# Performance work log

Measured on AMD Instinct MI355X. Metric: run time of the kernel, lower is better.

The kernel has to match this reference:

```python
import jax, jax.numpy as jnp
import numpy as np

BATCH, DIM, DB_SIZE, TOP_K = 2048, 512, 50000, 5

def setup_inputs() -> dict:
    key = jax.random.key(0)
    k1, k2 = jax.random.split(key)
    h_current = jax.random.normal(k1, (BATCH, DIM), dtype=jnp.float32)
    history_db = jax.random.normal(k2, (DB_SIZE, DIM), dtype=jnp.float32) * 0.01
    alpha = jnp.float32(0.5)
    return {"h_current": h_current, "history_db": history_db, "alpha": alpha, "top_k": TOP_K}

def _l2_normalize(x, eps=1e-12):
    # matches F.normalize(p=2): x / max(||x||, eps)
    n = jnp.linalg.norm(x, axis=-1, keepdims=True)
    return x / jnp.maximum(n, eps)

def reference(h_current, history_db, alpha, top_k):
    h_norm = _l2_normalize(h_current)            # (B, D)
    db_norm = _l2_normalize(history_db)          # (M, D)
    similarity = h_norm @ db_norm.T              # (B, M)
    topk_sim, topk_idx = jax.lax.top_k(similarity, top_k)  # (B, K)
    mu = jax.nn.softmax(topk_sim, axis=-1)       # (B, K)
    topk_embeddings = history_db[topk_idx]       # (B, K, D)
    h_retrieved = jnp.einsum('bk,bkd->bd', mu, topk_embeddings)
    a = jax.nn.sigmoid(alpha)
    return a * h_current + (1.0 - a) * h_retrieved
```

## Files before the change

### kernel.cpp

```cpp
#include <hip/hip_runtime.h>

#define BATCH   2048
#define DIM     512
#define DB_N    50000
#define TOPK    5
#define PADN    50176
#define NCHUNK  56
#define CTILES  7
#define CCOLS   896
#define TM      128
#define TN      128
#define NFIN    12

typedef float f32x4 __attribute__((ext_vector_type(4)));
typedef long long i64;
typedef long long i64x2 __attribute__((ext_vector_type(2)));

__device__ __forceinline__ void async16(const void* g, void* l) {
    __builtin_amdgcn_global_load_lds(
        (const __attribute__((address_space(1))) unsigned int*)g,
        (__attribute__((address_space(3))) unsigned int*)l, 16, 0, 0);
}

__device__ __forceinline__ unsigned sortbits(float v) {
    const int u = __float_as_int(v);
    return (unsigned)(u ^ ((u >> 31) | 0x80000000));
}

template<int NROWS>
__global__ void convert_kernel(const float* __restrict__ src, unsigned char* __restrict__ dst,
                               float* __restrict__ invp, int nreal) {
    const int r    = blockIdx.x * 4 + (threadIdx.x >> 6);
    const int lane = threadIdx.x & 63;
    float4 a = {0,0,0,0}, b = {0,0,0,0};
    float ss = 0.f;
    if (r < nreal) {
        const float* row = src + (size_t)r * DIM;
        a = *(const float4*)(row + lane * 8);
        b = *(const float4*)(row + lane * 8 + 4);
        ss = a.x*a.x + a.y*a.y + a.z*a.z + a.w*a.w
           + b.x*b.x + b.y*b.y + b.z*b.z + b.w*b.w;
    }
    #pragma unroll
    for (int off = 1; off < 64; off <<= 1) ss += __shfl_xor(ss, off);
    const float inv = 1.0f / fmaxf(sqrtf(ss), 1e-12f);
    const float s16 = inv * 16.0f;
    int lo = __builtin_amdgcn_cvt_pk_fp8_f32(a.x * s16, a.y * s16, 0, false);
    lo     = __builtin_amdgcn_cvt_pk_fp8_f32(a.z * s16, a.w * s16, lo, true);
    int hi = __builtin_amdgcn_cvt_pk_fp8_f32(b.x * s16, b.y * s16, 0, false);
    hi     = __builtin_amdgcn_cvt_pk_fp8_f32(b.z * s16, b.w * s16, hi, true);
    const int kb   = lane >> 4;
    const int q    = lane & 15;
    const int ks   = q >> 2;
    const int lh   = q & 3;
    const int u    = lh * 2 + (ks >> 1);
    const int half = ks & 1;
    int2 u2; u2.x = lo; u2.y = hi;
    *(int2*)(dst + ((size_t)kb * NROWS + r) * 128 + ((u ^ (r & 7)) << 4) + (half << 3)) = u2;
    if (invp && lane == 0) invp[r] = inv;
}

__global__ __launch_bounds__(512, 4) void sim_topk_kernel(
    const unsigned char* __restrict__ hzf, const unsigned char* __restrict__ dbzf,
    unsigned* __restrict__ pc) {

    __shared__ __align__(16) unsigned char As[2][TM * 128];
    __shared__ __align__(16) unsigned char Bs[2][TN * 128];
    __shared__ unsigned mrg[2][4][64][TOPK];

    const int tid  = threadIdx.x;
    const int lane = tid & 63;
    const int l15  = lane & 15;
    const int lhi  = lane >> 4;
    const int wid  = tid >> 6;
    const int uw   = __builtin_amdgcn_readfirstlane(wid);
    const int wm   = wid >> 2;
    const int wn   = wid & 3;
    const int mc   = blockIdx.x % NCHUNK;
    const int rb   = blockIdx.x / NCHUNK;
    const int c0   = mc * CCOLS;

    unsigned k0[16], k1[16];
    #pragma unroll
    for (int q = 0; q < 16; ++q) { k0[q] = 0u; k1[q] = 0u; }

    const int x7 = l15 & 7;
    const int aoff0 = (wm * 64 + l15) * 128 + ((((lhi << 1) | 0) ^ x7) << 4);
    const int aoff1 = (wm * 64 + l15) * 128 + ((((lhi << 1) | 1) ^ x7) << 4);
    const int boff0 = (wn * 32 + l15) * 128 + ((((lhi << 1) | 0) ^ x7) << 4);
    const int boff1 = (wn * 32 + l15) * 128 + ((((lhi << 1) | 1) ^ x7) << 4);

    auto STAGE = [&](int buf, int t, int kb) {
        const unsigned char* ga = hzf +
            (((size_t)kb * BATCH + (size_t)rb * TM) * 8 + uw * 128 + lane) * 16;
        const unsigned char* gb = dbzf +
            (((size_t)kb * PADN + (size_t)(c0 + t * TN)) * 8 + uw * 128 + lane) * 16;
        async16(ga,        &As[buf][uw * 2048]);
        async16(ga + 1024, &As[buf][uw * 2048 + 1024]);
        async16(gb,        &Bs[buf][uw * 2048]);
        async16(gb + 1024, &Bs[buf][uw * 2048 + 1024]);
    };

    f32x4 acc[4][2];

    STAGE(0, 0, 0);

    int p = 0;
    #pragma unroll 1
    for (int t = 0; t < CTILES; ++t) {
        #pragma unroll
        for (int mf = 0; mf < 4; ++mf)
            #pragma unroll
            for (int nf = 0; nf < 2; ++nf) acc[mf][nf] = (f32x4){0.f, 0.f, 0.f, 0.f};

        #pragma unroll
        for (int kb = 0; kb < 4; ++kb) {
            const int np = p + 1;
            if (np < CTILES * 4) {
                STAGE(np & 1, np >> 2, np & 3);
                asm volatile("s_waitcnt vmcnt(4)" ::: "memory");
            } else {
                asm volatile("s_waitcnt vmcnt(0)" ::: "memory");
            }
            __builtin_amdgcn_s_barrier();
            __builtin_amdgcn_sched_barrier(0);

            const unsigned char* ta = As[p & 1];
            const unsigned char* tb = Bs[p & 1];
            #pragma unroll
            for (int j = 0; j < 2; ++j) {
                const int ao = j ? aoff1 : aoff0;
                const int bo = j ? boff1 : boff0;
                i64x2 av[4], bv[2];
                #pragma unroll
                for (int mf = 0; mf < 4; ++mf)
                    av[mf] = *(const i64x2*)(ta + ao + mf * 2048);
                #pragma unroll
                for (int nf = 0; nf < 2; ++nf)
                    bv[nf] = *(const i64x2*)(tb + bo + nf * 2048);
                __builtin_amdgcn_s_setprio(1);
                #pragma unroll
                for (int hf = 0; hf < 2; ++hf)
                    #pragma unroll
                    for (int mf = 0; mf < 4; ++mf)
                        #pragma unroll
                        for (int nf = 0; nf < 2; ++nf)
                            acc[mf][nf] = __builtin_amdgcn_mfma_f32_16x16x32_fp8_fp8(
                                av[mf][hf], bv[nf][hf], acc[mf][nf], 0, 0, 0);
                __builtin_amdgcn_s_setprio(0);
            }
            __builtin_amdgcn_sched_barrier(0);
            __builtin_amdgcn_s_barrier();
            ++p;
        }

        const int tc = c0 + t * TN;
        #pragma unroll
        for (int nf = 0; nf < 2; ++nf) {
            const int  gcol  = tc + wn * 32 + nf * 16 + l15;
            const bool valid = gcol < DB_N;
            #pragma unroll
            for (int mf = 0; mf < 4; ++mf)
                #pragma unroll
                for (int i = 0; i < 4; ++i) {
                    const int q = mf * 4 + i;
                    const unsigned key = valid
                        ? ((sortbits(acc[mf][nf][i]) & 0xFFFF0000u) | (unsigned)gcol) : 0u;
                    const unsigned hi2 = key > k0[q] ? key   : k0[q];
                    const unsigned lo2 = key > k0[q] ? k0[q] : key;
                    k1[q] = lo2 > k1[q] ? lo2 : k1[q];
                    k0[q] = hi2;
                }
        }
    }

    #pragma unroll
    for (int mf = 0; mf < 4; ++mf)
        #pragma unroll
        for (int i = 0; i < 4; ++i) {
            const int q = mf * 4 + i;
            unsigned a0 = k0[q], a1 = k1[q];
            #pragma unroll
            for (int it = 0; it < TOPK; ++it) {
                unsigned w = a0;
                #pragma unroll
                for (int sh = 1; sh < 16; sh <<= 1) {
                    const unsigned o = (unsigned)__shfl_xor((int)w, sh);
                    w = o > w ? o : w;
                }
                const bool own = (a0 == w) && (w != 0u);
                a0 = own ? a1 : a0;
                a1 = own ? 0u : a1;
                if (l15 == q) mrg[wm][wn][mf * 16 + lhi * 4 + i][it] = w;
            }
        }
    __syncthreads();

    if (wn == 0) {
        unsigned bv[TOPK] = {0u, 0u, 0u, 0u, 0u};
        #pragma unroll
        for (int qq = 0; qq < 4; ++qq)
            #pragma unroll
            for (int j = 0; j < TOPK; ++j) {
                const unsigned u = mrg[wm][qq][lane][j];
                #pragma unroll
                for (int k = TOPK - 1; k >= 1; --k) {
                    const bool gt  = u > bv[k];
                    const bool gtp = u > bv[k - 1];
                    bv[k] = gt ? (gtp ? bv[k - 1] : u) : bv[k];
                }
                if (u > bv[0]) bv[0] = u;
            }
        const int row = rb * TM + wm * 64 + lane;
        #pragma unroll
        for (int j = 0; j < TOPK; ++j)
            pc[((size_t)row * NCHUNK + mc) * TOPK + j] = bv[j];
    }
}

__global__ void finalize_kernel(const float* __restrict__ h, const float* __restrict__ db,
                                const float* __restrict__ alpha_p,
                                const unsigned* __restrict__ pc,
                                const float* __restrict__ inv_db,
                                float* __restrict__ out) {
    const int b    = blockIdx.x;
    const int tid  = threadIdx.x;
    const int lane = tid & 63;
    const int wv   = tid >> 6;
    const int NC   = NCHUNK * TOPK;

    __shared__ int   fid[NFIN];
    __shared__ float fsim[NFIN];
    __shared__ float invh_s;
    __shared__ float mu_s[TOPK];
    __shared__ int   id_s[TOPK];

    if (wv == 0) {
        const unsigned* cp = pc + (size_t)b * NC;
        unsigned v[5];
        #pragma unroll
        for (int j = 0; j < 5; ++j) {
            const int c = lane + j * 64;
            v[j] = (c < NC) ? cp[c] : 0u;
        }
        for (int it = 0; it < NFIN; ++it) {
            unsigned m = v[0];
            #pragma unroll
            for (int j = 1; j < 5; ++j) m = v[j] > m ? v[j] : m;
            #pragma unroll
            for (int sh = 1; sh < 64; sh <<= 1) {
                const unsigned o = (unsigned)__shfl_xor((int)m, sh);
                m = o > m ? o : m;
            }
            if (lane == 0) {
                int gi = (int)(m & 0xFFFFu);
                fid[it] = gi < DB_N ? gi : DB_N - 1;
            }
            #pragma unroll
            for (int j = 0; j < 5; ++j) if (v[j] == m) v[j] = 0u;
        }
    } else if (wv == 1) {
        const float* hr = h + (size_t)b * DIM;
        const float4 a = *(const float4*)(hr + lane * 8);
        const float4 c = *(const float4*)(hr + lane * 8 + 4);
        float ss = a.x*a.x + a.y*a.y + a.z*a.z + a.w*a.w
                 + c.x*c.x + c.y*c.y + c.z*c.z + c.w*c.w;
        #pragma unroll
        for (int off = 1; off < 64; off <<= 1) ss += __shfl_xor(ss, off);
        if (lane == 0) invh_s = 1.0f / fmaxf(sqrtf(ss), 1e-12f);
    }
    __syncthreads();

    const float* hr = h + (size_t)b * DIM;
    for (int f = wv; f < NFIN; f += 4) {
        const int gi = fid[f];
        const float* dr = db + (size_t)gi * DIM;
        const float4 ha = *(const float4*)(hr + lane * 8);
        const float4 hb = *(const float4*)(hr + lane * 8 + 4);
        const float4 da = *(const float4*)(dr + lane * 8);
        const float4 dc = *(const float4*)(dr + lane * 8 + 4);
        float d = ha.x*da.x + ha.y*da.y + ha.z*da.z + ha.w*da.w
                + hb.x*dc.x + hb.y*dc.y + hb.z*dc.z + hb.w*dc.w;
        #pragma unroll
        for (int off = 1; off < 64; off <<= 1) d += __shfl_xor(d, off);
        if (lane == 0) fsim[f] = d * invh_s * inv_db[gi];
    }
    __syncthreads();

    if (tid == 0) {
        bool used[NFIN];
        #pragma unroll
        for (int j = 0; j < NFIN; ++j) used[j] = false;
        float bv[TOPK]; int bi[TOPK];
        for (int it = 0; it < TOPK; ++it) {
            float m = -3.0e38f; int mj = 0, mi = 0x7fffffff;
            for (int j = 0; j < NFIN; ++j) {
                if (used[j]) continue;
                if (fsim[j] > m || (fsim[j] == m && fid[j] < mi)) {
                    m = fsim[j]; mj = j; mi = fid[j];
                }
            }
            used[mj] = true; bv[it] = m; bi[it] = mi;
        }
        float ssum = 0.f, w[TOPK];
        #pragma unroll
        for (int j = 0; j < TOPK; ++j) { w[j] = expf(bv[j] - bv[0]); ssum += w[j]; }
        #pragma unroll
        for (int j = 0; j < TOPK; ++j) { mu_s[j] = w[j] / ssum; id_s[j] = bi[j]; }
    }
    __syncthreads();

    const float a = 1.0f / (1.0f + expf(-alpha_p[0]));
    for (int d = tid; d < DIM; d += 256) {
        float r = 0.f;
        #pragma unroll
        for (int j = 0; j < TOPK; ++j) r += mu_s[j] * db[(size_t)id_s[j] * DIM + d];
        out[(size_t)b * DIM + d] = a * h[(size_t)b * DIM + d] + (1.f - a) * r;
    }
}

extern "C" void kernel_launch(void* const* d_in, const int* in_sizes, int n_in,
                              void* d_out, int out_size, void* d_ws, size_t ws_size,
                              hipStream_t stream) {
    const float* h     = (const float*)d_in[0];
    const float* db    = (const float*)d_in[1];
    const float* alpha = (const float*)d_in[2];
    float* out = (float*)d_out;

    const size_t dbzf_bytes = (size_t)PADN * DIM;
    const size_t hzf_bytes  = (size_t)BATCH * DIM;
    const size_t inv_bytes  = (size_t)PADN * 4;

    unsigned char* dbzf  = (unsigned char*)d_ws;
    unsigned char* hzf   = (unsigned char*)d_ws + dbzf_bytes;
    float*         invdb = (float*)((char*)d_ws + dbzf_bytes + hzf_bytes);
    unsigned*      pc    = (unsigned*)((char*)d_ws + dbzf_bytes + hzf_bytes + inv_bytes);

    convert_kernel<PADN><<<PADN / 4, 256, 0, stream>>>(db, dbzf, invdb, DB_N);
    convert_kernel<BATCH><<<BATCH / 4, 256, 0, stream>>>(h, hzf, nullptr, BATCH);
    sim_topk_kernel<<<16 * NCHUNK, 512, 0, stream>>>(hzf, dbzf, pc);
    finalize_kernel<<<BATCH, 256, 0, stream>>>(h, db, alpha, pc, invdb, out);
}
```

Before: 167.8 us.

## Use 4-wave blocks with 64x64 warp tiles and k-major fp8 tile layout

The similarity GEMM block drops from 8 waves to 4. Each wave now computes a 64x64 output tile (4x4 MFMA fragments) instead of 64x32, and the K loop uses 64-byte k-steps (8 per tile) instead of 128-byte ones. The fp8 conversion writes a new tile-contiguous layout that is split by k-slab, so each stage copies contiguous 8KB slabs and the XOR swizzle is gone. The aim is more MFMA work per LDS fragment load and a simpler address pattern. The cost is more accumulator registers, less latency hiding per block, twice as many barriers per tile, and possible LDS bank conflicts now that there is no swizzle.

```diff
diff --git a/kernel.cpp b/kernel.cpp
--- a/kernel.cpp
+++ b/kernel.cpp
@@ -5,11 +5,10 @@
 #define DB_N    50000
 #define TOPK    5
 #define PADN    50176
+#define NTILES  392
 #define NCHUNK  56
 #define CTILES  7
 #define CCOLS   896
-#define TM      128
-#define TN      128
 #define NFIN    12
 
 typedef float f32x4 __attribute__((ext_vector_type(4)));
@@ -30,6 +29,7 @@
 template<int NROWS>
 __global__ void convert_kernel(const float* __restrict__ src, unsigned char* __restrict__ dst,
                                float* __restrict__ invp, int nreal) {
+    constexpr int NT = NROWS / 128;
     const int r    = blockIdx.x * 4 + (threadIdx.x >> 6);
     const int lane = threadIdx.x & 63;
     float4 a = {0,0,0,0}, b = {0,0,0,0};
@@ -49,24 +49,22 @@
     lo     = __builtin_amdgcn_cvt_pk_fp8_f32(a.z * s16, a.w * s16, lo, true);
     int hi = __builtin_amdgcn_cvt_pk_fp8_f32(b.x * s16, b.y * s16, 0, false);
     hi     = __builtin_amdgcn_cvt_pk_fp8_f32(b.z * s16, b.w * s16, hi, true);
-    const int kb   = lane >> 4;
-    const int q    = lane & 15;
-    const int ks   = q >> 2;
-    const int lh   = q & 3;
-    const int u    = lh * 2 + (ks >> 1);
-    const int half = ks & 1;
+    const int kb   = lane >> 3;
+    const int u    = lane & 3;
+    const int half = (lane >> 2) & 1;
     int2 u2; u2.x = lo; u2.y = hi;
-    *(int2*)(dst + ((size_t)kb * NROWS + r) * 128 + ((u ^ (r & 7)) << 4) + (half << 3)) = u2;
+    *(int2*)(dst + (((size_t)kb * NT + (r >> 7)) * 4 + u) * 2048
+                 + (r & 127) * 16 + (half << 3)) = u2;
     if (invp && lane == 0) invp[r] = inv;
 }
 
-__global__ __launch_bounds__(512, 4) void sim_topk_kernel(
+__global__ __launch_bounds__(256, 4) void sim_topk_kernel(
     const unsigned char* __restrict__ hzf, const unsigned char* __restrict__ dbzf,
     unsigned* __restrict__ pc) {
 
-    __shared__ __align__(16) unsigned char As[2][TM * 128];
-    __shared__ __align__(16) unsigned char Bs[2][TN * 128];
-    __shared__ unsigned mrg[2][4][64][TOPK];
+    __shared__ __align__(16) unsigned char As[2][8192];
+    __shared__ __align__(16) unsigned char Bs[2][8192];
+    __shared__ unsigned mrg[2][2][64][TOPK];
 
     const int tid  = threadIdx.x;
     const int lane = tid & 63;
@@ -74,8 +72,8 @@
     const int lhi  = lane >> 4;
     const int wid  = tid >> 6;
     const int uw   = __builtin_amdgcn_readfirstlane(wid);
-    const int wm   = wid >> 2;
-    const int wn   = wid & 3;
+    const int wm   = wid >> 1;
+    const int wn   = wid & 1;
     const int mc   = blockIdx.x % NCHUNK;
     const int rb   = blockIdx.x / NCHUNK;
     const int c0   = mc * CCOLS;
@@ -84,24 +82,20 @@
     #pragma unroll
     for (int q = 0; q < 16; ++q) { k0[q] = 0u; k1[q] = 0u; }
 
-    const int x7 = l15 & 7;
-    const int aoff0 = (wm * 64 + l15) * 128 + ((((lhi << 1) | 0) ^ x7) << 4);
-    const int aoff1 = (wm * 64 + l15) * 128 + ((((lhi << 1) | 1) ^ x7) << 4);
-    const int boff0 = (wn * 32 + l15) * 128 + ((((lhi << 1) | 0) ^ x7) << 4);
-    const int boff1 = (wn * 32 + l15) * 128 + ((((lhi << 1) | 1) ^ x7) << 4);
-
     auto STAGE = [&](int buf, int t, int kb) {
-        const unsigned char* ga = hzf +
-            (((size_t)kb * BATCH + (size_t)rb * TM) * 8 + uw * 128 + lane) * 16;
-        const unsigned char* gb = dbzf +
-            (((size_t)kb * PADN + (size_t)(c0 + t * TN)) * 8 + uw * 128 + lane) * 16;
-        async16(ga,        &As[buf][uw * 2048]);
-        async16(ga + 1024, &As[buf][uw * 2048 + 1024]);
-        async16(gb,        &Bs[buf][uw * 2048]);
-        async16(gb + 1024, &Bs[buf][uw * 2048 + 1024]);
+        const unsigned char* ga = hzf + (((size_t)kb * 16 + rb) << 13) + uw * 1024 + lane * 16;
+        const unsigned char* gb = dbzf + (((size_t)kb * NTILES + mc * CTILES + t) << 13)
+                                + uw * 1024 + lane * 16;
+        async16(ga,        &As[buf][uw * 1024]);
+        async16(ga + 4096, &As[buf][uw * 1024 + 4096]);
+        async16(gb,        &Bs[buf][uw * 1024]);
+        async16(gb + 4096, &Bs[buf][uw * 1024 + 4096]);
     };
 
-    f32x4 acc[4][2];
+    const int abase = lhi * 2048 + (wm * 64 + l15) * 16;
+    const int bbase = lhi * 2048 + (wn * 64 + l15) * 16;
+
+    f32x4 acc[4][4];
 
     STAGE(0, 0, 0);
 
@@ -111,13 +105,13 @@
         #pragma unroll
         for (int mf = 0; mf < 4; ++mf)
             #pragma unroll
-            for (int nf = 0; nf < 2; ++nf) acc[mf][nf] = (f32x4){0.f, 0.f, 0.f, 0.f};
-
-        #pragma unroll
-        for (int kb = 0; kb < 4; ++kb) {
+            for (int nf = 0; nf < 4; ++nf) acc[mf][nf] = (f32x4){0.f, 0.f, 0.f, 0.f};
+
+        #pragma unroll
+        for (int kb = 0; kb < 8; ++kb) {
             const int np = p + 1;
-            if (np < CTILES * 4) {
-                STAGE(np & 1, np >> 2, np & 3);
+            if (np < CTILES * 8) {
+                STAGE(np & 1, np >> 3, np & 7);
                 asm volatile("s_waitcnt vmcnt(4)" ::: "memory");
             } else {
                 asm volatile("s_waitcnt vmcnt(0)" ::: "memory");
@@ -127,37 +121,32 @@
 
             const unsigned char* ta = As[p & 1];
             const unsigned char* tb = Bs[p & 1];
-            #pragma unroll
-            for (int j = 0; j < 2; ++j) {
-                const int ao = j ? aoff1 : aoff0;
-                const int bo = j ? boff1 : boff0;
-                i64x2 av[4], bv[2];
+            i64x2 av[4], bv[4];
+            #pragma unroll
+            for (int mf = 0; mf < 4; ++mf)
+                av[mf] = *(const i64x2*)(ta + abase + mf * 256);
+            #pragma unroll
+            for (int nf = 0; nf < 4; ++nf)
+                bv[nf] = *(const i64x2*)(tb + bbase + nf * 256);
+            __builtin_amdgcn_s_setprio(1);
+            #pragma unroll
+            for (int hf = 0; hf < 2; ++hf)
                 #pragma unroll
                 for (int mf = 0; mf < 4; ++mf)
-                    av[mf] = *(const i64x2*)(ta + ao + mf * 2048);
-                #pragma unroll
-                for (int nf = 0; nf < 2; ++nf)
-                    bv[nf] = *(const i64x2*)(tb + bo + nf * 2048);
-                __builtin_amdgcn_s_setprio(1);
-                #pragma unroll
-                for (int hf = 0; hf < 2; ++hf)
                     #pragma unroll
-                    for (int mf = 0; mf < 4; ++mf)
-                        #pragma unroll
-                        for (int nf = 0; nf < 2; ++nf)
-                            acc[mf][nf] = __builtin_amdgcn_mfma_f32_16x16x32_fp8_fp8(
-                                av[mf][hf], bv[nf][hf], acc[mf][nf], 0, 0, 0);
-                __builtin_amdgcn_s_setprio(0);
-            }
+                    for (int nf = 0; nf < 4; ++nf)
+                        acc[mf][nf] = __builtin_amdgcn_mfma_f32_16x16x32_fp8_fp8(
+                            av[mf][hf], bv[nf][hf], acc[mf][nf], 0, 0, 0);
+            __builtin_amdgcn_s_setprio(0);
             __builtin_amdgcn_sched_barrier(0);
             __builtin_amdgcn_s_barrier();
             ++p;
         }
 
-        const int tc = c0 + t * TN;
-        #pragma unroll
-        for (int nf = 0; nf < 2; ++nf) {
-            const int  gcol  = tc + wn * 32 + nf * 16 + l15;
+        const int tc = c0 + t * 128;
+        #pragma unroll
+        for (int nf = 0; nf < 4; ++nf) {
+            const int  gcol  = tc + wn * 64 + nf * 16 + l15;
             const bool valid = gcol < DB_N;
             #pragma unroll
             for (int mf = 0; mf < 4; ++mf)
@@ -199,7 +188,7 @@
     if (wn == 0) {
         unsigned bv[TOPK] = {0u, 0u, 0u, 0u, 0u};
         #pragma unroll
-        for (int qq = 0; qq < 4; ++qq)
+        for (int qq = 0; qq < 2; ++qq)
             #pragma unroll
             for (int j = 0; j < TOPK; ++j) {
                 const unsigned u = mrg[wm][qq][lane][j];
@@ -211,7 +200,7 @@
                 }
                 if (u > bv[0]) bv[0] = u;
             }
-        const int row = rb * TM + wm * 64 + lane;
+        const int row = rb * 128 + wm * 64 + lane;
         #pragma unroll
         for (int j = 0; j < TOPK; ++j)
             pc[((size_t)row * NCHUNK + mc) * TOPK + j] = bv[j];
@@ -338,6 +327,6 @@
 
     convert_kernel<PADN><<<PADN / 4, 256, 0, stream>>>(db, dbzf, invdb, DB_N);
     convert_kernel<BATCH><<<BATCH / 4, 256, 0, stream>>>(h, hzf, nullptr, BATCH);
-    sim_topk_kernel<<<16 * NCHUNK, 512, 0, stream>>>(hzf, dbzf, pc);
+    sim_topk_kernel<<<16 * NCHUNK, 256, 0, stream>>>(hzf, dbzf, pc);
     finalize_kernel<<<BATCH, 256, 0, stream>>>(h, db, alpha, pc, invdb, out);
 }
```

Result: slower. 207.4 us (+23.6%).
